# Optimization experiments

Hardware: AMD Instinct MI355X
Metric: run time of the kernel (lower is better)

The kernel has to match this reference:

```python
import jax, jax.numpy as jnp
import numpy as np

B, L, D = 2, 4096, 512
H, HD = 8, 64  # num_heads, head_dim; H*HD == hidden_dim == 512


def setup_inputs() -> dict:
    key = jax.random.key(0)
    ks = jax.random.split(key, 12)
    s_in = 1.0 / np.sqrt(D)
    s_h = 1.0 / np.sqrt(H * HD)
    return {
        "query": jax.random.normal(ks[0], (B, L, D), jnp.float32),
        "key": jax.random.normal(ks[1], (B, L, D), jnp.float32),
        "value": jax.random.normal(ks[2], (B, L, D), jnp.float32),
        "mask": jnp.ones((B, L), jnp.int32),
        "Wq": jax.random.uniform(ks[3], (D, H * HD), jnp.float32, -s_in, s_in),
        "bq": jax.random.uniform(ks[4], (H * HD,), jnp.float32, -s_in, s_in),
        "Wk": jax.random.uniform(ks[5], (D, H * HD), jnp.float32, -s_in, s_in),
        "bk": jax.random.uniform(ks[6], (H * HD,), jnp.float32, -s_in, s_in),
        "Wv": jax.random.uniform(ks[7], (D, H * HD), jnp.float32, -s_in, s_in),
        "bv": jax.random.uniform(ks[8], (H * HD,), jnp.float32, -s_in, s_in),
        "Wo": jax.random.uniform(ks[9], (H * HD, D), jnp.float32, -s_h, s_h),
        "bo": jax.random.uniform(ks[10], (D,), jnp.float32, -s_h, s_h),
    }


def reference(query, key, value, mask, Wq, bq, Wk, bk, Wv, bv, Wo, bo):
    b, lq = query.shape[0], query.shape[1]
    lk = key.shape[1]
    # Linear projections, split heads: [B, H, L, HD]
    q = (query @ Wq + bq).reshape(b, lq, H, HD).transpose(0, 2, 1, 3)
    k = (key @ Wk + bk).reshape(b, lk, H, HD).transpose(0, 2, 1, 3)
    v = (value @ Wv + bv).reshape(b, lk, H, HD).transpose(0, 2, 1, 3)
    # scores: [B, H, Lq, Lk]
    scores = jnp.einsum("bhqd,bhkd->bhqk", q, k) / jnp.sqrt(jnp.float32(HD))
    m = mask[:, None, None, :]  # [B,1,1,Lk]
    scores = jnp.where(m == 0, jnp.float32(-jnp.inf), scores)
    attn = jax.nn.softmax(scores, axis=-1)
    # dropout is identity in eval / rate 0
    x = jnp.einsum("bhqk,bhkd->bhqd", attn, v)
    x = x.transpose(0, 2, 1, 3).reshape(b, lq, H * HD)
    return x @ Wo + bo
```

## Files before the change

kernel.cpp:

```cpp
#include <hip/hip_runtime.h>
#include <cmath>

typedef __attribute__((ext_vector_type(8))) __bf16 bf16x8;
typedef __attribute__((ext_vector_type(4))) __bf16 bf16x4;
typedef __attribute__((ext_vector_type(4))) float f32x4;
typedef __attribute__((ext_vector_type(2))) unsigned int u32x2;
typedef __attribute__((ext_vector_type(4))) unsigned int u32x4;

#define MFMA16(a, b, c) __builtin_amdgcn_mfma_f32_16x16x32_bf16(a, b, c, 0, 0, 0)

#define QSCALE 0.1803368801111601f

__device__ __forceinline__ void gload_lds16(void* lds, const void* g) {
    __builtin_amdgcn_global_load_lds(
        (const __attribute__((address_space(1))) unsigned int*)g,
        (__attribute__((address_space(3))) unsigned int*)lds, 16, 0, 0);
}

template <int PASSES>
__device__ __forceinline__ void stage_tile(char* lds, const __bf16* src,
                                           int stride_elems, int tid) {
    const char* s = (const char*)src;
    char* wbase = lds + (tid >> 6) * 1024;
#pragma unroll
    for (int p = 0; p < PASSES; ++p) {
        int i = p * 4096 + tid * 16;
        int row = i >> 7;
        int j = i ^ ((row & 7) << 4);
        gload_lds16(wbase + p * 4096,
                    s + (size_t)row * stride_elems * 2 + (j & 127));
    }
}

__device__ __forceinline__ bf16x8 frag_ld(const char* tile, int row, int kb) {
    int addr = (row << 7) + kb;
    addr ^= ((row & 7) << 4);
    return *(const bf16x8*)(tile + addr);
}

__global__ __launch_bounds__(256) void cast_x(const float* __restrict__ q,
                                              const float* __restrict__ k,
                                              const float* __restrict__ v,
                                              __bf16* __restrict__ X) {
    int z = blockIdx.z;
    const float* src = (z == 0) ? q : (z == 1) ? k : v;
    __bf16* dst = X + (size_t)z * 4194304;
    int i = blockIdx.x * 256 + threadIdx.x;
    float4 f = ((const float4*)src)[i];
    bf16x4 o = {(__bf16)f.x, (__bf16)f.y, (__bf16)f.z, (__bf16)f.w};
    ((bf16x4*)dst)[i] = o;
}

__global__ __launch_bounds__(256) void maskprep(const int* __restrict__ mask,
                                                float* __restrict__ mf) {
    int i = blockIdx.x * 256 + threadIdx.x;
    mf[i] = mask[i] ? 0.f : -1e30f;
}

__global__ __launch_bounds__(256) void wtrans(const float* __restrict__ Wq,
                                              const float* __restrict__ Wk,
                                              const float* __restrict__ Wv,
                                              const float* __restrict__ Wo,
                                              __bf16* __restrict__ Wt) {
    int z = blockIdx.z;
    const float* W = (z == 0) ? Wq : (z == 1) ? Wk : (z == 2) ? Wv : Wo;
    __bf16* out = Wt + (size_t)z * 262144;
    __shared__ float t[32][33];
    int r = threadIdx.x >> 5, cc = threadIdx.x & 31;
    int k0 = blockIdx.y * 32, n0 = blockIdx.x * 32;
#pragma unroll
    for (int rr = 0; rr < 4; ++rr)
        t[r + rr * 8][cc] = W[(size_t)(k0 + r + rr * 8) * 512 + n0 + cc];
    __syncthreads();
#pragma unroll
    for (int rr = 0; rr < 4; ++rr)
        out[(size_t)(n0 + r + rr * 8) * 512 + k0 + cc] = (__bf16)t[cc][r + rr * 8];
}

__global__ __launch_bounds__(256) void gemm_qkv(
    const __bf16* __restrict__ X, const __bf16* __restrict__ Wt,
    const float* __restrict__ b0, const float* __restrict__ b1,
    const float* __restrict__ b2, __bf16* __restrict__ Qo,
    __bf16* __restrict__ Ko, __bf16* __restrict__ Vto, int modeBase,
    float* __restrict__ outF) {
    __shared__ char smem[32768];
    char* At = smem;
    char* Bt = smem + 16384;
    int z = blockIdx.z;
    int mode = modeBase + z;
    const __bf16* A = X + (size_t)z * (8192 * 512);
    const __bf16* B = Wt + (size_t)z * (512 * 512);
    const float* bias = (mode == 1) ? b1 : (mode == 2) ? b2 : b0;

    int tid = threadIdx.x;
    int lane = tid & 63, wid = tid >> 6;
    int c = lane & 15, g = lane >> 4;
    int wm = (wid >> 1) * 64, wn = (wid & 1) * 64;
    int m0 = blockIdx.x * 128, n0 = blockIdx.y * 128;

    f32x4 zero = {0.f, 0.f, 0.f, 0.f};
    f32x4 acc[4][4];
#pragma unroll
    for (int i = 0; i < 4; ++i)
#pragma unroll
        for (int j = 0; j < 4; ++j) acc[i][j] = zero;

    for (int k0 = 0; k0 < 512; k0 += 64) {
        __syncthreads();
        stage_tile<4>(At, A + (size_t)m0 * 512 + k0, 512, tid);
        stage_tile<4>(Bt, B + (size_t)n0 * 512 + k0, 512, tid);
        __syncthreads();
#pragma unroll
        for (int ks = 0; ks < 2; ++ks) {
            bf16x8 af[4], bff[4];
#pragma unroll
            for (int mt = 0; mt < 4; ++mt)
                af[mt] = frag_ld(At, wm + mt * 16 + c, g * 16 + ks * 64);
#pragma unroll
            for (int nt = 0; nt < 4; ++nt)
                bff[nt] = frag_ld(Bt, wn + nt * 16 + c, g * 16 + ks * 64);
#pragma unroll
            for (int mt = 0; mt < 4; ++mt)
#pragma unroll
                for (int nt = 0; nt < 4; ++nt)
                    acc[mt][nt] = MFMA16(af[mt], bff[nt], acc[mt][nt]);
        }
    }

    float bv[4];
#pragma unroll
    for (int nt = 0; nt < 4; ++nt) bv[nt] = bias[n0 + wn + nt * 16 + c];
    float sc = (mode == 0) ? QSCALE : 1.0f;

    if (mode == 3) {
#pragma unroll
        for (int mt = 0; mt < 4; ++mt)
#pragma unroll
            for (int nt = 0; nt < 4; ++nt)
#pragma unroll
                for (int j = 0; j < 4; ++j) {
                    int m = m0 + wm + mt * 16 + g * 4 + j;
                    int n = n0 + wn + nt * 16 + c;
                    outF[(size_t)m * 512 + n] = acc[mt][nt][j] + bv[nt];
                }
    } else if (mode == 2) {
#pragma unroll
        for (int mt = 0; mt < 4; ++mt)
#pragma unroll
            for (int nt = 0; nt < 4; ++nt) {
                int m = m0 + wm + mt * 16 + g * 4;
                int n = n0 + wn + nt * 16 + c;
                int b = m >> 12, l = m & 4095, hh = n >> 6, hd = n & 63;
                bf16x4 v;
#pragma unroll
                for (int j = 0; j < 4; ++j)
                    v[j] = (__bf16)(acc[mt][nt][j] + bv[nt]);
                *(bf16x4*)(Vto + ((size_t)((b * 8 + hh) * 64 + hd)) * 4096 + l) = v;
            }
    } else {
        __bf16* dst = (mode == 0) ? Qo : Ko;
#pragma unroll
        for (int mt = 0; mt < 4; ++mt)
#pragma unroll
            for (int nt = 0; nt < 4; ++nt)
#pragma unroll
                for (int j = 0; j < 4; ++j) {
                    int m = m0 + wm + mt * 16 + g * 4 + j;
                    int n = n0 + wn + nt * 16 + c;
                    int b = m >> 12, l = m & 4095, hh = n >> 6, hd = n & 63;
                    dst[((size_t)((b * 8 + hh) * 4096 + l)) * 64 + hd] =
                        (__bf16)((acc[mt][nt][j] + bv[nt]) * sc);
                }
    }
}

__global__ __launch_bounds__(256) void attn_fa(const __bf16* __restrict__ Q,
                                               const __bf16* __restrict__ K,
                                               const __bf16* __restrict__ Vt,
                                               const float* __restrict__ mf,
                                               __bf16* __restrict__ O) {
    __shared__ char smem[65536];

    int tid = threadIdx.x, lane = tid & 63, wid = tid >> 6;
    int c = lane & 15, g = lane >> 4;

    int sw = (blockIdx.x & 7) * 64 + (blockIdx.x >> 3);
    int bh = sw >> 5, b = bh >> 3, h = bh & 7;
    int q0 = (sw & 31) * 128;

    const __bf16* Qb = Q + (size_t)bh * 4096 * 64;
    const __bf16* Kb = K + (size_t)bh * 4096 * 64;
    const __bf16* Vb = Vt + (size_t)bh * 64 * 4096;
    int qw = q0 + wid * 32;

    {
        const float4* msrc = (const float4*)(mf + (size_t)b * 4096);
        float4* mdst = (float4*)(smem + 49152);
#pragma unroll
        for (int p = 0; p < 4; ++p) mdst[p * 256 + tid] = msrc[p * 256 + tid];
    }

    bf16x8 qf[2][2];
#pragma unroll
    for (int nq = 0; nq < 2; ++nq)
#pragma unroll
        for (int ks = 0; ks < 2; ++ks)
            qf[nq][ks] = *(const bf16x8*)(Qb + (size_t)(qw + nq * 16 + c) * 64 +
                                          g * 8 + ks * 32);

    int rowp = tid >> 3;
    int jlow = ((tid & 7) << 4) ^ ((rowp & 7) << 4);
    const char* kB0 = (const char*)Kb + rowp * 128 + jlow;
    const char* kB1 = (const char*)Kb + (32 + rowp) * 128 + jlow;
    const char* vB0 = (const char*)Vb + rowp * 8192 + jlow;
    const char* vB1 = (const char*)Vb + (32 + rowp) * 8192 + jlow;
    int woff = (tid >> 6) * 1024;

#define STAGE(t)                                                         \
    {                                                                    \
        int u_ = (t) % 3;                                                \
        size_t ko_ = (size_t)(t) * 8192, vo_ = (size_t)(t) * 128;        \
        gload_lds16(smem + u_ * 8192 + woff, kB0 + ko_);                 \
        gload_lds16(smem + u_ * 8192 + 4096 + woff, kB1 + ko_);          \
        gload_lds16(smem + 24576 + u_ * 8192 + woff, vB0 + vo_);         \
        gload_lds16(smem + 24576 + u_ * 8192 + 4096 + woff, vB1 + vo_);  \
    }

    f32x4 zero = {0.f, 0.f, 0.f, 0.f};
    f32x4 acc[4][2];
#pragma unroll
    for (int i = 0; i < 4; ++i)
#pragma unroll
        for (int j = 0; j < 2; ++j) acc[i][j] = zero;
    f32x4 rsum4[2] = {zero, zero};

    STAGE(0);
    STAGE(1);

    for (int t = 0; t < 64; ++t) {
        if (t == 63)
            asm volatile("s_waitcnt vmcnt(0)" ::: "memory");
        else
            asm volatile("s_waitcnt vmcnt(4)" ::: "memory");
        __builtin_amdgcn_s_barrier();
        __builtin_amdgcn_sched_barrier(0);
        if (t < 62) STAGE(t + 2);

        int u = t % 3;
        const char* Ktc = smem + u * 8192;
        const char* Vtc = smem + 24576 + u * 8192;

        f32x4 s[4][2];
#pragma unroll
        for (int mt = 0; mt < 4; ++mt) {
            f32x4 mv =
                *(const f32x4*)(smem + 49152 + t * 256 + mt * 64 + g * 16);
            s[mt][0] = mv;
            s[mt][1] = mv;
        }

        __builtin_amdgcn_s_setprio(1);
#pragma unroll
        for (int ks = 0; ks < 2; ++ks) {
            bf16x8 kf[4];
#pragma unroll
            for (int mt = 0; mt < 4; ++mt)
                kf[mt] = frag_ld(Ktc, mt * 16 + c, g * 16 + ks * 64);
#pragma unroll
            for (int mt = 0; mt < 4; ++mt)
#pragma unroll
                for (int nq = 0; nq < 2; ++nq)
                    s[mt][nq] = MFMA16(kf[mt], qf[nq][ks], s[mt][nq]);
        }
        __builtin_amdgcn_s_setprio(0);

        unsigned int pku[4][2][2];
#pragma unroll
        for (int mt = 0; mt < 4; ++mt)
#pragma unroll
            for (int nq = 0; nq < 2; ++nq) {
                f32x4 p;
#pragma unroll
                for (int j = 0; j < 4; ++j)
                    p[j] = __builtin_amdgcn_exp2f(s[mt][nq][j]);
                rsum4[nq] += p;
                bf16x4 pw = {(__bf16)p[0], (__bf16)p[1], (__bf16)p[2],
                             (__bf16)p[3]};
                u32x2 u2 = __builtin_bit_cast(u32x2, pw);
                pku[mt][nq][0] = u2.x;
                pku[mt][nq][1] = u2.y;
            }

#pragma unroll
        for (int ks2 = 0; ks2 < 2; ++ks2) {
            bf16x8 vf[4];
#pragma unroll
            for (int mh = 0; mh < 4; ++mh)
                vf[mh] = frag_ld(Vtc, mh * 16 + c, g * 16 + ks2 * 64);
            bf16x8 pf[2];
#pragma unroll
            for (int nq = 0; nq < 2; ++nq) {
                unsigned int a0 = pku[2 * ks2][nq][0];
                unsigned int a1 = pku[2 * ks2][nq][1];
                unsigned int b0 = pku[2 * ks2 + 1][nq][0];
                unsigned int b1 = pku[2 * ks2 + 1][nq][1];
                asm("v_permlane32_swap_b32 %0, %1" : "+v"(a0), "+v"(b0));
                asm("v_permlane32_swap_b32 %0, %1" : "+v"(a1), "+v"(b1));
                asm("v_permlane16_swap_b32 %0, %1" : "+v"(a0), "+v"(b0));
                asm("v_permlane16_swap_b32 %0, %1" : "+v"(a1), "+v"(b1));
                u32x4 pv = {a0, a1, b0, b1};
                pf[nq] = __builtin_bit_cast(bf16x8, pv);
            }
            __builtin_amdgcn_s_setprio(1);
#pragma unroll
            for (int mh = 0; mh < 4; ++mh)
#pragma unroll
                for (int nq = 0; nq < 2; ++nq)
                    acc[mh][nq] = MFMA16(vf[mh], pf[nq], acc[mh][nq]);
            __builtin_amdgcn_s_setprio(0);
        }
    }
#undef STAGE

    float rl[2];
#pragma unroll
    for (int nq = 0; nq < 2; ++nq) {
        float r = (rsum4[nq][0] + rsum4[nq][1]) + (rsum4[nq][2] + rsum4[nq][3]);
        r += __shfl_xor(r, 16, 64);
        r += __shfl_xor(r, 32, 64);
        rl[nq] = 1.0f / r;
    }

    __syncthreads();

    char* Pw = smem + wid * 4608;
#pragma unroll
    for (int mh = 0; mh < 4; ++mh)
#pragma unroll
        for (int nq = 0; nq < 2; ++nq) {
            bf16x4 o;
#pragma unroll
            for (int j = 0; j < 4; ++j) o[j] = (__bf16)(acc[mh][nq][j] * rl[nq]);
            *(bf16x4*)(Pw + (nq * 16 + c) * 144 + mh * 32 + g * 8) = o;
        }
    __syncthreads();
#pragma unroll
    for (int p = 0; p < 4; ++p) {
        int i = p * 4096 + tid * 16;
        int row = i >> 7, colb = i & 127;
        bf16x8 v = *(const bf16x8*)(smem + row * 144 + colb);
        *(bf16x8*)(O + ((size_t)(b * 4096 + q0 + row)) * 512 + h * 64 +
                   colb / 2) = v;
    }
}

extern "C" void kernel_launch(void* const* d_in, const int* in_sizes, int n_in,
                              void* d_out, int out_size, void* d_ws,
                              size_t ws_size, hipStream_t stream) {
    const float* query = (const float*)d_in[0];
    const float* key = (const float*)d_in[1];
    const float* value = (const float*)d_in[2];
    const int* mask = (const int*)d_in[3];
    const float* Wq = (const float*)d_in[4];
    const float* bq = (const float*)d_in[5];
    const float* Wk = (const float*)d_in[6];
    const float* bk = (const float*)d_in[7];
    const float* Wv = (const float*)d_in[8];
    const float* bv = (const float*)d_in[9];
    const float* Wo = (const float*)d_in[10];
    const float* bo = (const float*)d_in[11];

    char* ws = (char*)d_ws;
    __bf16* Xbf = (__bf16*)(ws);
    __bf16* Wt = (__bf16*)(ws + 25165824);
    __bf16* Qb = (__bf16*)(ws + 27262976);
    __bf16* Kb = (__bf16*)(ws + 35651584);
    __bf16* Vtb = (__bf16*)(ws + 44040192);
    __bf16* Ob = (__bf16*)(ws + 52428800);
    float* mfb = (float*)Xbf;

    cast_x<<<dim3(4096, 1, 3), 256, 0, stream>>>(query, key, value, Xbf);
    wtrans<<<dim3(16, 16, 4), 256, 0, stream>>>(Wq, Wk, Wv, Wo, Wt);
    gemm_qkv<<<dim3(64, 4, 3), 256, 0, stream>>>(Xbf, Wt, bq, bk, bv, Qb, Kb,
                                                 Vtb, 0, nullptr);
    maskprep<<<dim3(32), 256, 0, stream>>>(mask, mfb);
    attn_fa<<<dim3(512), 256, 0, stream>>>(Qb, Kb, Vtb, mfb, Ob);
    gemm_qkv<<<dim3(64, 4, 1), 256, 0, stream>>>(Ob, Wt + 3 * 262144, bo, bo,
                                                 bo, Qb, Kb, Vtb, 3,
                                                 (float*)d_out);
}
```

Measured before the change: 150.8 us.

## Software-pipeline QK^T of next tile with softmax-PV of current tile; fuse mask prep

Restructures the attention inner loop so the QK^T MFMAs for tile t+1 are issued before the exp/PV work of tile t, ping-ponging two score register sets. The K ring stays three-deep and the V ring grows to four-deep with prefetch distance 3, which raises LDS use to 72KB and may reduce occupancy. The separate maskprep kernel is removed and the int mask is converted to the additive float mask inside attn_fa, saving one launch. Waits are now vmcnt(0) at every step, which may reduce how much load latency is hidden.

Measured after the change: 141.4 us, median of 2. -6.2%, faster.

```diff
diff --git a/kernel.cpp b/kernel.cpp
--- a/kernel.cpp
+++ b/kernel.cpp
@@ -49,12 +49,6 @@
     float4 f = ((const float4*)src)[i];
     bf16x4 o = {(__bf16)f.x, (__bf16)f.y, (__bf16)f.z, (__bf16)f.w};
     ((bf16x4*)dst)[i] = o;
-}
-
-__global__ __launch_bounds__(256) void maskprep(const int* __restrict__ mask,
-                                                float* __restrict__ mf) {
-    int i = blockIdx.x * 256 + threadIdx.x;
-    mf[i] = mask[i] ? 0.f : -1e30f;
 }
 
 __global__ __launch_bounds__(256) void wtrans(const float* __restrict__ Wq,
@@ -177,9 +171,9 @@
 __global__ __launch_bounds__(256) void attn_fa(const __bf16* __restrict__ Q,
                                                const __bf16* __restrict__ K,
                                                const __bf16* __restrict__ Vt,
-                                               const float* __restrict__ mf,
+                                               const int* __restrict__ mask,
                                                __bf16* __restrict__ O) {
-    __shared__ char smem[65536];
+    __shared__ char smem[73728];
 
     int tid = threadIdx.x, lane = tid & 63, wid = tid >> 6;
     int c = lane & 15, g = lane >> 4;
@@ -194,10 +188,15 @@
     int qw = q0 + wid * 32;
 
     {
-        const float4* msrc = (const float4*)(mf + (size_t)b * 4096);
-        float4* mdst = (float4*)(smem + 49152);
-#pragma unroll
-        for (int p = 0; p < 4; ++p) mdst[p * 256 + tid] = msrc[p * 256 + tid];
+        const int4* msrc = (const int4*)(mask + (size_t)b * 4096);
+        float4* mdst = (float4*)(smem + 57344);
+#pragma unroll
+        for (int p = 0; p < 4; ++p) {
+            int4 m = msrc[p * 256 + tid];
+            float4 f = {m.x ? 0.f : -1e30f, m.y ? 0.f : -1e30f,
+                        m.z ? 0.f : -1e30f, m.w ? 0.f : -1e30f};
+            mdst[p * 256 + tid] = f;
+        }
     }
 
     bf16x8 qf[2][2];
@@ -216,14 +215,14 @@
     const char* vB1 = (const char*)Vb + (32 + rowp) * 8192 + jlow;
     int woff = (tid >> 6) * 1024;
 
-#define STAGE(t)                                                         \
-    {                                                                    \
-        int u_ = (t) % 3;                                                \
-        size_t ko_ = (size_t)(t) * 8192, vo_ = (size_t)(t) * 128;        \
-        gload_lds16(smem + u_ * 8192 + woff, kB0 + ko_);                 \
-        gload_lds16(smem + u_ * 8192 + 4096 + woff, kB1 + ko_);          \
-        gload_lds16(smem + 24576 + u_ * 8192 + woff, vB0 + vo_);         \
-        gload_lds16(smem + 24576 + u_ * 8192 + 4096 + woff, vB1 + vo_);  \
+#define STAGE(t)                                                              \
+    {                                                                         \
+        int uk_ = (t) % 3, uv_ = (t) & 3;                                     \
+        size_t ko_ = (size_t)(t) * 8192, vo_ = (size_t)(t) * 128;             \
+        gload_lds16(smem + uk_ * 8192 + woff, kB0 + ko_);                     \
+        gload_lds16(smem + uk_ * 8192 + 4096 + woff, kB1 + ko_);              \
+        gload_lds16(smem + 24576 + uv_ * 8192 + woff, vB0 + vo_);             \
+        gload_lds16(smem + 24576 + uv_ * 8192 + 4096 + woff, vB1 + vo_);      \
     }
 
     f32x4 zero = {0.f, 0.f, 0.f, 0.f};
@@ -234,31 +233,15 @@
         for (int j = 0; j < 2; ++j) acc[i][j] = zero;
     f32x4 rsum4[2] = {zero, zero};
 
-    STAGE(0);
-    STAGE(1);
-
-    for (int t = 0; t < 64; ++t) {
-        if (t == 63)
-            asm volatile("s_waitcnt vmcnt(0)" ::: "memory");
-        else
-            asm volatile("s_waitcnt vmcnt(4)" ::: "memory");
-        __builtin_amdgcn_s_barrier();
-        __builtin_amdgcn_sched_barrier(0);
-        if (t < 62) STAGE(t + 2);
-
-        int u = t % 3;
-        const char* Ktc = smem + u * 8192;
-        const char* Vtc = smem + 24576 + u * 8192;
-
-        f32x4 s[4][2];
+    auto QKT = [&](int t, f32x4(&s)[4][2]) {
+        const char* Ktc = smem + (t % 3) * 8192;
 #pragma unroll
         for (int mt = 0; mt < 4; ++mt) {
             f32x4 mv =
-                *(const f32x4*)(smem + 49152 + t * 256 + mt * 64 + g * 16);
+                *(const f32x4*)(smem + 57344 + t * 256 + mt * 64 + g * 16);
             s[mt][0] = mv;
             s[mt][1] = mv;
         }
-
         __builtin_amdgcn_s_setprio(1);
 #pragma unroll
         for (int ks = 0; ks < 2; ++ks) {
@@ -273,7 +256,10 @@
                     s[mt][nq] = MFMA16(kf[mt], qf[nq][ks], s[mt][nq]);
         }
         __builtin_amdgcn_s_setprio(0);
-
+    };
+
+    auto SMPV = [&](int t, f32x4(&s)[4][2]) {
+        const char* Vtc = smem + 24576 + (t & 3) * 8192;
         unsigned int pku[4][2][2];
 #pragma unroll
         for (int mt = 0; mt < 4; ++mt)
@@ -290,7 +276,6 @@
                 pku[mt][nq][0] = u2.x;
                 pku[mt][nq][1] = u2.y;
             }
-
 #pragma unroll
         for (int ks2 = 0; ks2 < 2; ++ks2) {
             bf16x8 vf[4];
@@ -319,6 +304,35 @@
                     acc[mh][nq] = MFMA16(vf[mh], pf[nq], acc[mh][nq]);
             __builtin_amdgcn_s_setprio(0);
         }
+    };
+
+    asm volatile("s_waitcnt vmcnt(0) lgkmcnt(0)" ::: "memory");
+    __builtin_amdgcn_sched_barrier(0);
+    STAGE(0);
+    STAGE(1);
+    STAGE(2);
+    asm volatile("s_waitcnt vmcnt(8)" ::: "memory");
+    __builtin_amdgcn_s_barrier();
+    __builtin_amdgcn_sched_barrier(0);
+
+    f32x4 sA[4][2], sB[4][2];
+    QKT(0, sA);
+
+#pragma unroll 1
+    for (int tt = 0; tt < 32; ++tt) {
+        int t0 = 2 * tt, t1 = 2 * tt + 1;
+        asm volatile("s_waitcnt vmcnt(0)" ::: "memory");
+        __builtin_amdgcn_s_barrier();
+        __builtin_amdgcn_sched_barrier(0);
+        if (t0 <= 60) STAGE(t0 + 3);
+        if (t0 < 63) QKT(t0 + 1, sB);
+        SMPV(t0, sA);
+        asm volatile("s_waitcnt vmcnt(0)" ::: "memory");
+        __builtin_amdgcn_s_barrier();
+        __builtin_amdgcn_sched_barrier(0);
+        if (t1 <= 60) STAGE(t1 + 3);
+        if (t1 < 63) QKT(t1 + 1, sA);
+        SMPV(t1, sB);
     }
 #undef STAGE
 
@@ -377,14 +391,12 @@
     __bf16* Kb = (__bf16*)(ws + 35651584);
     __bf16* Vtb = (__bf16*)(ws + 44040192);
     __bf16* Ob = (__bf16*)(ws + 52428800);
-    float* mfb = (float*)Xbf;
 
     cast_x<<<dim3(4096, 1, 3), 256, 0, stream>>>(query, key, value, Xbf);
     wtrans<<<dim3(16, 16, 4), 256, 0, stream>>>(Wq, Wk, Wv, Wo, Wt);
     gemm_qkv<<<dim3(64, 4, 3), 256, 0, stream>>>(Xbf, Wt, bq, bk, bv, Qb, Kb,
                                                  Vtb, 0, nullptr);
-    maskprep<<<dim3(32), 256, 0, stream>>>(mask, mfb);
-    attn_fa<<<dim3(512), 256, 0, stream>>>(Qb, Kb, Vtb, mfb, Ob);
+    attn_fa<<<dim3(512), 256, 0, stream>>>(Qb, Kb, Vtb, mask, Ob);
     gemm_qkv<<<dim3(64, 4, 1), 256, 0, stream>>>(Ob, Wt + 3 * 262144, bo, bo,
                                                  bo, Qb, Kb, Vtb, 3,
                                                  (float*)d_out);
```

## Software-pipeline QK^T one tile ahead of softmax-PV and load mask from global

Applied to the files above, without the earlier changes.

Restructures the attention main loop so the QK^T MFMAs for tile t+1 are issued before the softmax and PV work for tile t, ping-ponging two score register sets. K buffers drop to double buffering while V stays triple-buffered. Mask values are now read straight from global into registers two tiles ahead instead of being staged into LDS, which shrinks shared memory from 64KB to 40KB and may allow higher occupancy. The cost is more live registers for the second score set and __syncthreads that now rely on the compiler's waitcnt rather than explicit vmcnt control.

Result: slower. 195.4 us (+29.6%).

```diff
diff --git a/kernel.cpp b/kernel.cpp
--- a/kernel.cpp
+++ b/kernel.cpp
@@ -179,7 +179,7 @@
                                                const __bf16* __restrict__ Vt,
                                                const float* __restrict__ mf,
                                                __bf16* __restrict__ O) {
-    __shared__ char smem[65536];
+    __shared__ char smem[40960];
 
     int tid = threadIdx.x, lane = tid & 63, wid = tid >> 6;
     int c = lane & 15, g = lane >> 4;
@@ -191,14 +191,8 @@
     const __bf16* Qb = Q + (size_t)bh * 4096 * 64;
     const __bf16* Kb = K + (size_t)bh * 4096 * 64;
     const __bf16* Vb = Vt + (size_t)bh * 64 * 4096;
+    const float* mfb = mf + (size_t)b * 4096;
     int qw = q0 + wid * 32;
-
-    {
-        const float4* msrc = (const float4*)(mf + (size_t)b * 4096);
-        float4* mdst = (float4*)(smem + 49152);
-#pragma unroll
-        for (int p = 0; p < 4; ++p) mdst[p * 256 + tid] = msrc[p * 256 + tid];
-    }
 
     bf16x8 qf[2][2];
 #pragma unroll
@@ -216,14 +210,14 @@
     const char* vB1 = (const char*)Vb + (32 + rowp) * 8192 + jlow;
     int woff = (tid >> 6) * 1024;
 
-#define STAGE(t)                                                         \
-    {                                                                    \
-        int u_ = (t) % 3;                                                \
-        size_t ko_ = (size_t)(t) * 8192, vo_ = (size_t)(t) * 128;        \
-        gload_lds16(smem + u_ * 8192 + woff, kB0 + ko_);                 \
-        gload_lds16(smem + u_ * 8192 + 4096 + woff, kB1 + ko_);          \
-        gload_lds16(smem + 24576 + u_ * 8192 + woff, vB0 + vo_);         \
-        gload_lds16(smem + 24576 + u_ * 8192 + 4096 + woff, vB1 + vo_);  \
+#define STAGE(t)                                                              \
+    {                                                                         \
+        int uk_ = (t) & 1, uv_ = (t) % 3;                                     \
+        size_t ko_ = (size_t)(t) * 8192, vo_ = (size_t)(t) * 128;             \
+        gload_lds16(smem + uk_ * 8192 + woff, kB0 + ko_);                     \
+        gload_lds16(smem + uk_ * 8192 + 4096 + woff, kB1 + ko_);              \
+        gload_lds16(smem + 16384 + uv_ * 8192 + woff, vB0 + vo_);             \
+        gload_lds16(smem + 16384 + uv_ * 8192 + 4096 + woff, vB1 + vo_);      \
     }
 
     f32x4 zero = {0.f, 0.f, 0.f, 0.f};
@@ -234,31 +228,19 @@
         for (int j = 0; j < 2; ++j) acc[i][j] = zero;
     f32x4 rsum4[2] = {zero, zero};
 
-    STAGE(0);
-    STAGE(1);
-
-    for (int t = 0; t < 64; ++t) {
-        if (t == 63)
-            asm volatile("s_waitcnt vmcnt(0)" ::: "memory");
-        else
-            asm volatile("s_waitcnt vmcnt(4)" ::: "memory");
-        __builtin_amdgcn_s_barrier();
-        __builtin_amdgcn_sched_barrier(0);
-        if (t < 62) STAGE(t + 2);
-
-        int u = t % 3;
-        const char* Ktc = smem + u * 8192;
-        const char* Vtc = smem + 24576 + u * 8192;
-
-        f32x4 s[4][2];
+    auto LDMASK = [&](int t, f32x4(&mv)[4]) {
+#pragma unroll
+        for (int mt = 0; mt < 4; ++mt)
+            mv[mt] = *(const f32x4*)(mfb + t * 64 + mt * 16 + g * 4);
+    };
+
+    auto QKT = [&](int t, f32x4(&s)[4][2], const f32x4(&mv)[4]) {
+        const char* Ktc = smem + (t & 1) * 8192;
 #pragma unroll
         for (int mt = 0; mt < 4; ++mt) {
-            f32x4 mv =
-                *(const f32x4*)(smem + 49152 + t * 256 + mt * 64 + g * 16);
-            s[mt][0] = mv;
-            s[mt][1] = mv;
-        }
-
+            s[mt][0] = mv[mt];
+            s[mt][1] = mv[mt];
+        }
         __builtin_amdgcn_s_setprio(1);
 #pragma unroll
         for (int ks = 0; ks < 2; ++ks) {
@@ -273,7 +255,10 @@
                     s[mt][nq] = MFMA16(kf[mt], qf[nq][ks], s[mt][nq]);
         }
         __builtin_amdgcn_s_setprio(0);
-
+    };
+
+    auto SMPV = [&](int t, f32x4(&s)[4][2]) {
+        const char* Vtc = smem + 16384 + (t % 3) * 8192;
         unsigned int pku[4][2][2];
 #pragma unroll
         for (int mt = 0; mt < 4; ++mt)
@@ -290,7 +275,6 @@
                 pku[mt][nq][0] = u2.x;
                 pku[mt][nq][1] = u2.y;
             }
-
 #pragma unroll
         for (int ks2 = 0; ks2 < 2; ++ks2) {
             bf16x8 vf[4];
@@ -319,6 +303,35 @@
                     acc[mh][nq] = MFMA16(vf[mh], pf[nq], acc[mh][nq]);
             __builtin_amdgcn_s_setprio(0);
         }
+    };
+
+    f32x4 mvA[4], mvB[4];
+    STAGE(0);
+    STAGE(1);
+    LDMASK(0, mvA);
+    LDMASK(1, mvB);
+    __syncthreads();
+
+    f32x4 sA[4][2], sB[4][2];
+    QKT(0, sA, mvA);
+
+#pragma unroll 1
+    for (int tt = 0; tt < 32; ++tt) {
+        int t0 = 2 * tt, t1 = 2 * tt + 1;
+        __syncthreads();
+        if (t0 <= 61) {
+            STAGE(t0 + 2);
+            LDMASK(t0 + 2, mvA);
+        }
+        if (t0 < 63) QKT(t0 + 1, sB, mvB);
+        SMPV(t0, sA);
+        __syncthreads();
+        if (t1 <= 61) {
+            STAGE(t1 + 2);
+            LDMASK(t1 + 2, mvB);
+        }
+        if (t1 < 63) QKT(t1 + 1, sA, mvA);
+        SMPV(t1, sB);
     }
 #undef STAGE
 
```
